# Kernel tuning notes

Hardware: AMD Instinct MI355X
Metric: run time of the kernel (lower is better)

## Reference

```python
import jax, jax.numpy as jnp
import numpy as np

B, S, D, E, K = 4, 2048, 1024, 8, 2
H = 4 * D  # FFN hidden per expert


def setup_inputs() -> dict:
    key = jax.random.key(0)
    ks = jax.random.split(key, 5)
    s = 0.02  # init scale
    return {
        "x": jax.random.normal(ks[0], (B, S, D), dtype=jnp.float32),
        "Wg": jax.random.normal(ks[1], (D, E), dtype=jnp.float32) * s,
        "bg": jnp.zeros((E,), dtype=jnp.float32),
        "W1": jax.random.normal(ks[2], (E, D, H), dtype=jnp.float32) * s,
        "b1": jnp.zeros((E, H), dtype=jnp.float32),
        "W2": jax.random.normal(ks[3], (E, H, D), dtype=jnp.float32) * s,
        "b2": jnp.zeros((E, D), dtype=jnp.float32),
    }


def reference(x, Wg, bg, W1, b1, W2, b2):
    # Router: softmax over expert logits, then top-k (torch.topk semantics)
    probs = jax.nn.softmax(x @ Wg + bg, axis=-1)      # [B,S,E]
    w, idx = jax.lax.top_k(probs, K)                   # [B,S,K] each
    # Dense all-experts MLP (matches original: every expert runs on every token)
    h = jax.nn.gelu(jnp.einsum('bsd,edh->bseh', x, W1) + b1, approximate=False)  # [B,S,E,H]
    y = jnp.einsum('bseh,ehd->bsed', h, W2) + b2       # [B,S,E,D]
    # One-hot mask + weighted sum == gather selected experts, scale by w, sum over k
    yk = jnp.take_along_axis(y, idx[..., None], axis=2)  # [B,S,K,D]
    return jnp.sum(yk * w[..., None], axis=2)            # [B,S,D]
```

## Files before the change

kernel.cpp:

```cpp
#include <hip/hip_runtime.h>
#include <hip/hip_bf16.h>
#include <math.h>


#define TOK     8192
#define DMODEL  1024
#define NEXP    8
#define HFF     4096
#define NASSIGN 16384
#define SLOTPAD 16512
#define BM      128
#define BN      128
#define BK      64
#define MAXRT   135

typedef __attribute__((ext_vector_type(8))) short s16x8;
typedef __attribute__((ext_vector_type(4))) float f32x4;

__device__ __forceinline__ void gll16(const void* g, void* l) {
  __builtin_amdgcn_global_load_lds((const __attribute__((address_space(1))) void*)g,
                                   (__attribute__((address_space(3))) void*)l, 16, 0, 0);
}

__global__ void transpose_cvt(const float* __restrict__ in, __hip_bfloat16* __restrict__ out,
                              int R, int C) {
  __shared__ float t[64][65];
  const float* src = in + (size_t)blockIdx.z * R * C;
  __hip_bfloat16* dst = out + (size_t)blockIdx.z * R * C;
  const int r0 = blockIdx.y * 64, c0 = blockIdx.x * 64;
  const int tc = threadIdx.x & 63, tr = threadIdx.x >> 6;
#pragma unroll
  for (int i = 0; i < 16; ++i) {
    int r = i * 4 + tr;
    t[r][tc] = src[(size_t)(r0 + r) * C + c0 + tc];
  }
  __syncthreads();
  const int jl = (threadIdx.x & 15) * 4;
  const int cw = threadIdx.x >> 4;
#pragma unroll
  for (int p = 0; p < 4; ++p) {
    const int cc = p * 16 + cw;
    union { ushort4 u; __hip_bfloat16 h[4]; } o;
#pragma unroll
    for (int u = 0; u < 4; ++u) o.h[u] = __float2bfloat16(t[jl + u][cc]);
    *(ushort4*)(dst + (size_t)(c0 + cc) * R + r0 + jl) = o.u;
  }
}

__global__ void router_kernel(const float* __restrict__ x, const float* __restrict__ Wg,
                              const float* __restrict__ bg, int* __restrict__ idx,
                              float* __restrict__ wtok, int* __restrict__ counts) {
  __shared__ int scnt[NEXP];
  if (threadIdx.x < NEXP) scnt[threadIdx.x] = 0;
  __syncthreads();
  const int wave = threadIdx.x >> 6, lane = threadIdx.x & 63;
  const int t = blockIdx.x * 4 + wave;
  float acc[NEXP];
#pragma unroll
  for (int e = 0; e < NEXP; ++e) acc[e] = 0.f;
  const float* xr = x + (size_t)t * DMODEL + lane * 16;
#pragma unroll
  for (int j = 0; j < 4; ++j) {
    float4 xv = *(const float4*)(xr + j * 4);
    const float* wr = Wg + (size_t)(lane * 16 + j * 4) * NEXP;
#pragma unroll
    for (int u = 0; u < 4; ++u) {
      float xs = (&xv.x)[u];
      float4 w0 = *(const float4*)(wr + u * NEXP);
      float4 w1 = *(const float4*)(wr + u * NEXP + 4);
      acc[0] += xs * w0.x; acc[1] += xs * w0.y; acc[2] += xs * w0.z; acc[3] += xs * w0.w;
      acc[4] += xs * w1.x; acc[5] += xs * w1.y; acc[6] += xs * w1.z; acc[7] += xs * w1.w;
    }
  }
#pragma unroll
  for (int off = 32; off >= 1; off >>= 1) {
#pragma unroll
    for (int e = 0; e < NEXP; ++e) acc[e] += __shfl_xor(acc[e], off, 64);
  }
  if (lane == 0) {
    float l[NEXP], m = -1e30f;
#pragma unroll
    for (int e = 0; e < NEXP; ++e) { l[e] = acc[e] + bg[e]; m = fmaxf(m, l[e]); }
    float p[NEXP], s = 0.f;
#pragma unroll
    for (int e = 0; e < NEXP; ++e) { p[e] = expf(l[e] - m); s += p[e]; }
    float inv = 1.f / s;
#pragma unroll
    for (int e = 0; e < NEXP; ++e) p[e] *= inv;
    int i0 = 0; float v0 = p[0];
#pragma unroll
    for (int e = 1; e < NEXP; ++e) if (p[e] > v0) { v0 = p[e]; i0 = e; }
    int i1 = -1; float v1 = -1e30f;
#pragma unroll
    for (int e = 0; e < NEXP; ++e) if (e != i0 && p[e] > v1) { v1 = p[e]; i1 = e; }
    idx[2 * t] = i0; idx[2 * t + 1] = i1;
    wtok[2 * t] = v0; wtok[2 * t + 1] = v1;
    atomicAdd(&scnt[i0], 1); atomicAdd(&scnt[i1], 1);
  }
  __syncthreads();
  if (threadIdx.x < NEXP) atomicAdd(&counts[threadIdx.x], scnt[threadIdx.x]);
}

__global__ void scan_kernel(int* ctrl) {
  if (threadIdx.x == 0 && blockIdx.x == 0) {
    int* counts = ctrl;
    int* cursor = ctrl + 8;
    int* expOff = ctrl + 16;
    int* tro = ctrl + 26;
    expOff[0] = 0; tro[0] = 0;
    for (int e = 0; e < NEXP; ++e) {
      expOff[e + 1] = expOff[e] + counts[e];
      tro[e + 1] = tro[e] + (counts[e] + BM - 1) / BM;
      cursor[e] = expOff[e];
    }
  }
}

__global__ void scatter_kernel(const int* __restrict__ idx, const float* __restrict__ wtok,
                               int* ctrl, int* __restrict__ perm, float* __restrict__ wslot) {
  __shared__ int lcnt[NEXP];
  __shared__ int lbase[NEXP];
  const int t = blockIdx.x * 256 + threadIdx.x;
  if (threadIdx.x < NEXP) lcnt[threadIdx.x] = 0;
  __syncthreads();
  const int e0 = idx[2 * t], e1 = idx[2 * t + 1];
  const int l0 = atomicAdd(&lcnt[e0], 1);
  const int l1 = atomicAdd(&lcnt[e1], 1);
  __syncthreads();
  if (threadIdx.x < NEXP)
    lbase[threadIdx.x] = atomicAdd(&ctrl[8 + threadIdx.x], lcnt[threadIdx.x]);
  __syncthreads();
  const int s0 = lbase[e0] + l0, s1 = lbase[e1] + l1;
  perm[s0] = t; perm[s1] = t;
  wslot[s0] = wtok[2 * t]; wslot[s1] = wtok[2 * t + 1];
}

__global__ void gather_cvt_x(const float* __restrict__ x, const int* __restrict__ perm,
                             __hip_bfloat16* __restrict__ xg) {
  const int slot = blockIdx.x;
  const int t = perm[slot];
  const float4 v = *(const float4*)(x + (size_t)t * DMODEL + threadIdx.x * 4);
  union { ushort4 u; __hip_bfloat16 h[4]; } o;
  o.h[0] = __float2bfloat16(v.x); o.h[1] = __float2bfloat16(v.y);
  o.h[2] = __float2bfloat16(v.z); o.h[3] = __float2bfloat16(v.w);
  *(ushort4*)(xg + (size_t)slot * DMODEL + threadIdx.x * 4) = o.u;
}


__global__ __launch_bounds__(256, 3) void gemm1_kernel(
    const __hip_bfloat16* __restrict__ xg, const __hip_bfloat16* __restrict__ w1t,
    const float* __restrict__ b1, __hip_bfloat16* __restrict__ hbuf,
    const int* __restrict__ ctrl) {
  const int* expOff = ctrl + 16;
  const int* tro = ctrl + 26;
  const int w = blockIdx.x;
  const int rt = w >> 5, nt = w & 31;
  if (rt >= tro[NEXP]) return;
  int e = 0;
#pragma unroll
  for (int q = 1; q < NEXP; ++q) if (tro[q] <= rt) e = q;
  const int rowBase = expOff[e] + (rt - tro[e]) * BM;
  const int rowEnd = expOff[e + 1];

  __shared__ __hip_bfloat16 lA[BM * BK];
  __shared__ __hip_bfloat16 lB[BN * BK];

  const int tid = threadIdx.x;
  const int lane = tid & 63, wave = tid >> 6;
  const int quad = lane >> 4, lm = lane & 15;
  const int waveM = (wave >> 1) * 64, waveN = (wave & 1) * 64;

  f32x4 acc[4][4];
#pragma unroll
  for (int a = 0; a < 4; ++a)
#pragma unroll
    for (int b = 0; b < 4; ++b) acc[a][b] = (f32x4){0.f, 0.f, 0.f, 0.f};

  const __hip_bfloat16* bbase = w1t + (size_t)e * HFF * DMODEL + (size_t)nt * BN * DMODEL;
  const __hip_bfloat16* gA[4]; const __hip_bfloat16* gB[4];
  __hip_bfloat16* sA[4]; __hip_bfloat16* sB[4];
#pragma unroll
  for (int i = 0; i < 4; ++i) {
    const int s = tid + 256 * i;
    const int r = s >> 3, sl = s & 7, kc = sl ^ (r & 7);
    gA[i] = xg + (size_t)(rowBase + r) * DMODEL + kc * 8;
    gB[i] = bbase + (size_t)r * DMODEL + kc * 8;
    sA[i] = lA + s * 8; sB[i] = lB + s * 8;
  }

  int aOff[4], bOff[4];
#pragma unroll
  for (int tm = 0; tm < 4; ++tm) {
    int r = waveM + tm * 16 + lm;
    aOff[tm] = r * 64 + (quad ^ (r & 7)) * 8;
  }
#pragma unroll
  for (int tn = 0; tn < 4; ++tn) {
    int r = waveN + tn * 16 + lm;
    bOff[tn] = r * 64 + (quad ^ (r & 7)) * 8;
  }

  for (int kt = 0; kt < DMODEL / BK; ++kt) {
#pragma unroll
    for (int i = 0; i < 4; ++i) { gll16(gA[i], sA[i]); gll16(gB[i], sB[i]); }
#pragma unroll
    for (int i = 0; i < 4; ++i) { gA[i] += BK; gB[i] += BK; }
    __syncthreads();
#pragma unroll
    for (int h = 0; h < 2; ++h) {
      s16x8 af[4], bfr[4];
#pragma unroll
      for (int tm = 0; tm < 4; ++tm) af[tm] = *(const s16x8*)(lA + (aOff[tm] ^ (h * 32)));
#pragma unroll
      for (int tn = 0; tn < 4; ++tn) bfr[tn] = *(const s16x8*)(lB + (bOff[tn] ^ (h * 32)));
#pragma unroll
      for (int tm = 0; tm < 4; ++tm)
#pragma unroll
        for (int tn = 0; tn < 4; ++tn)
          acc[tm][tn] = __builtin_amdgcn_mfma_f32_16x16x32_bf16(af[tm], bfr[tn], acc[tm][tn], 0, 0, 0);
    }
    __syncthreads();
  }

  const int colBase = nt * BN + waveN;
  float bv[4];
#pragma unroll
  for (int tn = 0; tn < 4; ++tn) bv[tn] = b1[e * HFF + colBase + tn * 16 + lm];
#pragma unroll
  for (int tm = 0; tm < 4; ++tm) {
    const int rb = rowBase + waveM + tm * 16 + quad * 4;
#pragma unroll
    for (int reg = 0; reg < 4; ++reg) {
      const int row = rb + reg;
      if (row < rowEnd) {
#pragma unroll
        for (int tn = 0; tn < 4; ++tn) {
          float v = acc[tm][tn][reg] + bv[tn];
          v = 0.5f * v * (1.f + erff(v * 0.70710678118654752f));
          hbuf[(size_t)row * HFF + colBase + tn * 16 + lm] = __float2bfloat16(v);
        }
      }
    }
  }
}

__global__ __launch_bounds__(256, 3) void gemm2_kernel(
    const __hip_bfloat16* __restrict__ hbuf, const __hip_bfloat16* __restrict__ w2t,
    const float* __restrict__ b2, const float* __restrict__ wslot,
    const int* __restrict__ perm, float* __restrict__ out, const int* __restrict__ ctrl) {
  const int* expOff = ctrl + 16;
  const int* tro = ctrl + 26;
  const int w = blockIdx.x;
  const int rt = w >> 3, nt = w & 7;
  if (rt >= tro[NEXP]) return;
  int e = 0;
#pragma unroll
  for (int q = 1; q < NEXP; ++q) if (tro[q] <= rt) e = q;
  const int rowBase = expOff[e] + (rt - tro[e]) * BM;
  const int rowEnd = expOff[e + 1];

  __shared__ __hip_bfloat16 lA[BM * BK];
  __shared__ __hip_bfloat16 lB[BN * BK];

  const int tid = threadIdx.x;
  const int lane = tid & 63, wave = tid >> 6;
  const int quad = lane >> 4, lm = lane & 15;
  const int waveM = (wave >> 1) * 64, waveN = (wave & 1) * 64;

  f32x4 acc[4][4];
#pragma unroll
  for (int a = 0; a < 4; ++a)
#pragma unroll
    for (int b = 0; b < 4; ++b) acc[a][b] = (f32x4){0.f, 0.f, 0.f, 0.f};

  const __hip_bfloat16* bbase = w2t + (size_t)e * DMODEL * HFF + (size_t)nt * BN * HFF;
  const __hip_bfloat16* gA[4]; const __hip_bfloat16* gB[4];
  __hip_bfloat16* sA[4]; __hip_bfloat16* sB[4];
#pragma unroll
  for (int i = 0; i < 4; ++i) {
    const int s = tid + 256 * i;
    const int r = s >> 3, sl = s & 7, kc = sl ^ (r & 7);
    gA[i] = hbuf + (size_t)(rowBase + r) * HFF + kc * 8;
    gB[i] = bbase + (size_t)r * HFF + kc * 8;
    sA[i] = lA + s * 8; sB[i] = lB + s * 8;
  }

  int aOff[4], bOff[4];
#pragma unroll
  for (int tm = 0; tm < 4; ++tm) {
    int r = waveM + tm * 16 + lm;
    aOff[tm] = r * 64 + (quad ^ (r & 7)) * 8;
  }
#pragma unroll
  for (int tn = 0; tn < 4; ++tn) {
    int r = waveN + tn * 16 + lm;
    bOff[tn] = r * 64 + (quad ^ (r & 7)) * 8;
  }

  for (int kt = 0; kt < HFF / BK; ++kt) {
#pragma unroll
    for (int i = 0; i < 4; ++i) { gll16(gA[i], sA[i]); gll16(gB[i], sB[i]); }
#pragma unroll
    for (int i = 0; i < 4; ++i) { gA[i] += BK; gB[i] += BK; }
    __syncthreads();
#pragma unroll
    for (int h = 0; h < 2; ++h) {
      s16x8 af[4], bfr[4];
#pragma unroll
      for (int tm = 0; tm < 4; ++tm) af[tm] = *(const s16x8*)(lA + (aOff[tm] ^ (h * 32)));
#pragma unroll
      for (int tn = 0; tn < 4; ++tn) bfr[tn] = *(const s16x8*)(lB + (bOff[tn] ^ (h * 32)));
#pragma unroll
      for (int tm = 0; tm < 4; ++tm)
#pragma unroll
        for (int tn = 0; tn < 4; ++tn)
          acc[tm][tn] = __builtin_amdgcn_mfma_f32_16x16x32_bf16(af[tm], bfr[tn], acc[tm][tn], 0, 0, 0);
    }
    __syncthreads();
  }

  const int colBase = nt * BN + waveN;
  float bv[4];
#pragma unroll
  for (int tn = 0; tn < 4; ++tn) bv[tn] = b2[e * DMODEL + colBase + tn * 16 + lm];
#pragma unroll
  for (int tm = 0; tm < 4; ++tm) {
    const int rb = rowBase + waveM + tm * 16 + quad * 4;
#pragma unroll
    for (int reg = 0; reg < 4; ++reg) {
      const int row = rb + reg;
      if (row < rowEnd) {
        const float wr = wslot[row];
        float* orow = out + (size_t)perm[row] * DMODEL + colBase;
#pragma unroll
        for (int tn = 0; tn < 4; ++tn)
          atomicAdd(orow + tn * 16 + lm, (acc[tm][tn][reg] + bv[tn]) * wr);
      }
    }
  }
}

extern "C" void kernel_launch(void* const* d_in, const int* in_sizes, int n_in,
                              void* d_out, int out_size, void* d_ws, size_t ws_size,
                              hipStream_t stream) {
  const float* x  = (const float*)d_in[0];
  const float* Wg = (const float*)d_in[1];
  const float* bg = (const float*)d_in[2];
  const float* W1 = (const float*)d_in[3];
  const float* b1 = (const float*)d_in[4];
  const float* W2 = (const float*)d_in[5];
  const float* b2 = (const float*)d_in[6];
  float* out = (float*)d_out;

  char* ws = (char*)d_ws;
  size_t off = 0;
  auto take = [&](size_t bytes) -> char* {
    char* p = ws + off;
    off = (off + bytes + 255) & ~(size_t)255;
    return p;
  };
  int*   ctrl  = (int*)take(64 * sizeof(int));
  int*   idx   = (int*)take((size_t)TOK * 2 * 4);
  float* wtok  = (float*)take((size_t)TOK * 2 * 4);
  int*   perm  = (int*)take((size_t)SLOTPAD * 4);
  float* wslot = (float*)take((size_t)SLOTPAD * 4);
  __hip_bfloat16* W1t = (__hip_bfloat16*)take((size_t)NEXP * HFF * DMODEL * 2);
  __hip_bfloat16* W2t = (__hip_bfloat16*)take((size_t)NEXP * DMODEL * HFF * 2);
  __hip_bfloat16* xgb = (__hip_bfloat16*)take((size_t)SLOTPAD * DMODEL * 2);
  __hip_bfloat16* hb  = (__hip_bfloat16*)take((size_t)SLOTPAD * HFF * 2);
  (void)ws_size; (void)in_sizes; (void)n_in; (void)out_size;

  hipMemsetAsync(ctrl, 0, 64 * sizeof(int), stream);
  hipMemsetAsync(out, 0, (size_t)TOK * DMODEL * 4, stream);
  transpose_cvt<<<dim3(HFF / 64, DMODEL / 64, NEXP), 256, 0, stream>>>(W1, W1t, DMODEL, HFF);
  transpose_cvt<<<dim3(DMODEL / 64, HFF / 64, NEXP), 256, 0, stream>>>(W2, W2t, HFF, DMODEL);
  router_kernel<<<TOK / 4, 256, 0, stream>>>(x, Wg, bg, idx, wtok, ctrl);
  scan_kernel<<<1, 64, 0, stream>>>(ctrl);
  scatter_kernel<<<TOK / 256, 256, 0, stream>>>(idx, wtok, ctrl, perm, wslot);
  gather_cvt_x<<<NASSIGN, 256, 0, stream>>>(x, perm, xgb);
  gemm1_kernel<<<MAXRT * (HFF / BN), 256, 0, stream>>>(xgb, W1t, b1, hb, ctrl);
  gemm2_kernel<<<MAXRT * (DMODEL / BN), 256, 0, stream>>>(hb, W2t, b2, wslot, perm, out, ctrl);
}
```

Measured before the change: 793.5 us.

## Double-buffer GEMM LDS tiles, fuse launches, replace atomic combine with gather

Both grouped GEMMs now double-buffer their LDS tiles. The next K-tile is prefetched while MFMAs run on the current one, with one barrier per iteration and raised wave priority during the MFMA burst. The two weight transposes merge into one launch, and the scan is folded into the router through a last-block-done counter. Gemm2 now writes weighted per-slot rows to a scratch buffer that aliases W1t, and a new combine kernel sums the two slots per token. This removes the output memset and the float atomics. It costs extra LDS (occupancy bound drops to 2) plus an extra pass over the slot outputs.

Result: slower. 982.0 us (+23.8%).

```diff
diff --git a/kernel.cpp b/kernel.cpp
--- a/kernel.cpp
+++ b/kernel.cpp
@@ -22,12 +22,21 @@
                                    (__attribute__((address_space(3))) void*)l, 16, 0, 0);
 }
 
-__global__ void transpose_cvt(const float* __restrict__ in, __hip_bfloat16* __restrict__ out,
-                              int R, int C) {
+__global__ void transpose_cvt(const float* __restrict__ W1, const float* __restrict__ W2,
+                              __hip_bfloat16* __restrict__ W1t, __hip_bfloat16* __restrict__ W2t) {
   __shared__ float t[64][65];
-  const float* src = in + (size_t)blockIdx.z * R * C;
-  __hip_bfloat16* dst = out + (size_t)blockIdx.z * R * C;
-  const int r0 = blockIdx.y * 64, c0 = blockIdx.x * 64;
+  const int z = blockIdx.y;
+  const float* src; __hip_bfloat16* dst; int R, C, bx, by;
+  if (z < 8) {
+    R = DMODEL; C = HFF;
+    src = W1 + (size_t)z * R * C; dst = W1t + (size_t)z * R * C;
+    bx = blockIdx.x & 63; by = blockIdx.x >> 6;
+  } else {
+    R = HFF; C = DMODEL;
+    src = W2 + (size_t)(z - 8) * R * C; dst = W2t + (size_t)(z - 8) * R * C;
+    bx = blockIdx.x & 15; by = blockIdx.x >> 4;
+  }
+  const int r0 = by * 64, c0 = bx * 64;
   const int tc = threadIdx.x & 63, tr = threadIdx.x >> 6;
 #pragma unroll
   for (int i = 0; i < 16; ++i) {
@@ -49,7 +58,7 @@
 
 __global__ void router_kernel(const float* __restrict__ x, const float* __restrict__ Wg,
                               const float* __restrict__ bg, int* __restrict__ idx,
-                              float* __restrict__ wtok, int* __restrict__ counts) {
+                              float* __restrict__ wtok, int* ctrl) {
   __shared__ int scnt[NEXP];
   if (threadIdx.x < NEXP) scnt[threadIdx.x] = 0;
   __syncthreads();
@@ -98,26 +107,30 @@
     atomicAdd(&scnt[i0], 1); atomicAdd(&scnt[i1], 1);
   }
   __syncthreads();
-  if (threadIdx.x < NEXP) atomicAdd(&counts[threadIdx.x], scnt[threadIdx.x]);
-}
-
-__global__ void scan_kernel(int* ctrl) {
-  if (threadIdx.x == 0 && blockIdx.x == 0) {
-    int* counts = ctrl;
-    int* cursor = ctrl + 8;
-    int* expOff = ctrl + 16;
-    int* tro = ctrl + 26;
-    expOff[0] = 0; tro[0] = 0;
-    for (int e = 0; e < NEXP; ++e) {
-      expOff[e + 1] = expOff[e] + counts[e];
-      tro[e + 1] = tro[e] + (counts[e] + BM - 1) / BM;
-      cursor[e] = expOff[e];
+  if (threadIdx.x < NEXP) atomicAdd(&ctrl[threadIdx.x], scnt[threadIdx.x]);
+  if (threadIdx.x == 0) {
+    __threadfence();
+    const int done = atomicAdd(&ctrl[63], 1);
+    if (done == (int)gridDim.x - 1) {
+      int c[NEXP];
+#pragma unroll
+      for (int e = 0; e < NEXP; ++e) c[e] = atomicAdd(&ctrl[e], 0);
+      int eo = 0, tr = 0;
+      ctrl[16] = 0; ctrl[26] = 0;
+#pragma unroll
+      for (int e = 0; e < NEXP; ++e) {
+        ctrl[8 + e] = eo;
+        eo += c[e]; tr += (c[e] + BM - 1) / BM;
+        ctrl[17 + e] = eo;
+        ctrl[27 + e] = tr;
+      }
     }
   }
 }
 
 __global__ void scatter_kernel(const int* __restrict__ idx, const float* __restrict__ wtok,
-                               int* ctrl, int* __restrict__ perm, float* __restrict__ wslot) {
+                               int* ctrl, int* __restrict__ perm, int* __restrict__ ts,
+                               float* __restrict__ wslot) {
   __shared__ int lcnt[NEXP];
   __shared__ int lbase[NEXP];
   const int t = blockIdx.x * 256 + threadIdx.x;
@@ -132,6 +145,7 @@
   __syncthreads();
   const int s0 = lbase[e0] + l0, s1 = lbase[e1] + l1;
   perm[s0] = t; perm[s1] = t;
+  ts[2 * t] = s0; ts[2 * t + 1] = s1;
   wslot[s0] = wtok[2 * t]; wslot[s1] = wtok[2 * t + 1];
 }
 
@@ -147,7 +161,7 @@
 }
 
 
-__global__ __launch_bounds__(256, 3) void gemm1_kernel(
+__global__ __launch_bounds__(256, 2) void gemm1_kernel(
     const __hip_bfloat16* __restrict__ xg, const __hip_bfloat16* __restrict__ w1t,
     const float* __restrict__ b1, __hip_bfloat16* __restrict__ hbuf,
     const int* __restrict__ ctrl) {
@@ -162,8 +176,8 @@
   const int rowBase = expOff[e] + (rt - tro[e]) * BM;
   const int rowEnd = expOff[e + 1];
 
-  __shared__ __hip_bfloat16 lA[BM * BK];
-  __shared__ __hip_bfloat16 lB[BN * BK];
+  __shared__ __hip_bfloat16 lA[2 * BM * BK];
+  __shared__ __hip_bfloat16 lB[2 * BN * BK];
 
   const int tid = threadIdx.x;
   const int lane = tid & 63, wave = tid >> 6;
@@ -178,14 +192,12 @@
 
   const __hip_bfloat16* bbase = w1t + (size_t)e * HFF * DMODEL + (size_t)nt * BN * DMODEL;
   const __hip_bfloat16* gA[4]; const __hip_bfloat16* gB[4];
-  __hip_bfloat16* sA[4]; __hip_bfloat16* sB[4];
 #pragma unroll
   for (int i = 0; i < 4; ++i) {
     const int s = tid + 256 * i;
     const int r = s >> 3, sl = s & 7, kc = sl ^ (r & 7);
     gA[i] = xg + (size_t)(rowBase + r) * DMODEL + kc * 8;
     gB[i] = bbase + (size_t)r * DMODEL + kc * 8;
-    sA[i] = lA + s * 8; sB[i] = lB + s * 8;
   }
 
   int aOff[4], bOff[4];
@@ -200,26 +212,46 @@
     bOff[tn] = r * 64 + (quad ^ (r & 7)) * 8;
   }
 
-  for (int kt = 0; kt < DMODEL / BK; ++kt) {
-#pragma unroll
-    for (int i = 0; i < 4; ++i) { gll16(gA[i], sA[i]); gll16(gB[i], sB[i]); }
-#pragma unroll
-    for (int i = 0; i < 4; ++i) { gA[i] += BK; gB[i] += BK; }
-    __syncthreads();
+#pragma unroll
+  for (int i = 0; i < 4; ++i) {
+    gll16(gA[i], lA + tid * 8 + i * 2048);
+    gll16(gB[i], lB + tid * 8 + i * 2048);
+    gA[i] += BK; gB[i] += BK;
+  }
+  __syncthreads();
+
+  const int NTI = DMODEL / BK;
+  for (int kt = 0; kt < NTI; ++kt) {
+    if (kt + 1 < NTI) {
+      const int nb = (kt + 1) & 1;
+#pragma unroll
+      for (int i = 0; i < 4; ++i) {
+        gll16(gA[i], lA + nb * 8192 + tid * 8 + i * 2048);
+        gll16(gB[i], lB + nb * 8192 + tid * 8 + i * 2048);
+        gA[i] += BK; gB[i] += BK;
+      }
+    }
+    const __hip_bfloat16* ba = lA + (kt & 1) * 8192;
+    const __hip_bfloat16* bb = lB + (kt & 1) * 8192;
+    s16x8 af[2][4], bfr[2][4];
 #pragma unroll
     for (int h = 0; h < 2; ++h) {
-      s16x8 af[4], bfr[4];
-#pragma unroll
-      for (int tm = 0; tm < 4; ++tm) af[tm] = *(const s16x8*)(lA + (aOff[tm] ^ (h * 32)));
-#pragma unroll
-      for (int tn = 0; tn < 4; ++tn) bfr[tn] = *(const s16x8*)(lB + (bOff[tn] ^ (h * 32)));
+#pragma unroll
+      for (int tm = 0; tm < 4; ++tm) af[h][tm] = *(const s16x8*)(ba + (aOff[tm] ^ (h * 32)));
+#pragma unroll
+      for (int tn = 0; tn < 4; ++tn) bfr[h][tn] = *(const s16x8*)(bb + (bOff[tn] ^ (h * 32)));
+    }
+    __builtin_amdgcn_s_setprio(1);
+#pragma unroll
+    for (int h = 0; h < 2; ++h)
 #pragma unroll
       for (int tm = 0; tm < 4; ++tm)
 #pragma unroll
         for (int tn = 0; tn < 4; ++tn)
-          acc[tm][tn] = __builtin_amdgcn_mfma_f32_16x16x32_bf16(af[tm], bfr[tn], acc[tm][tn], 0, 0, 0);
-    }
-    __syncthreads();
+          acc[tm][tn] = __builtin_amdgcn_mfma_f32_16x16x32_bf16(af[h][tm], bfr[h][tn],
+                                                                acc[tm][tn], 0, 0, 0);
+    __builtin_amdgcn_s_setprio(0);
+    if (kt + 1 < NTI) __syncthreads();
   }
 
   const int colBase = nt * BN + waveN;
@@ -244,10 +276,10 @@
   }
 }
 
-__global__ __launch_bounds__(256, 3) void gemm2_kernel(
+__global__ __launch_bounds__(256, 2) void gemm2_kernel(
     const __hip_bfloat16* __restrict__ hbuf, const __hip_bfloat16* __restrict__ w2t,
     const float* __restrict__ b2, const float* __restrict__ wslot,
-    const int* __restrict__ perm, float* __restrict__ out, const int* __restrict__ ctrl) {
+    float* __restrict__ y, const int* __restrict__ ctrl) {
   const int* expOff = ctrl + 16;
   const int* tro = ctrl + 26;
   const int w = blockIdx.x;
@@ -259,8 +291,8 @@
   const int rowBase = expOff[e] + (rt - tro[e]) * BM;
   const int rowEnd = expOff[e + 1];
 
-  __shared__ __hip_bfloat16 lA[BM * BK];
-  __shared__ __hip_bfloat16 lB[BN * BK];
+  __shared__ __hip_bfloat16 lA[2 * BM * BK];
+  __shared__ __hip_bfloat16 lB[2 * BN * BK];
 
   const int tid = threadIdx.x;
   const int lane = tid & 63, wave = tid >> 6;
@@ -275,14 +307,12 @@
 
   const __hip_bfloat16* bbase = w2t + (size_t)e * DMODEL * HFF + (size_t)nt * BN * HFF;
   const __hip_bfloat16* gA[4]; const __hip_bfloat16* gB[4];
-  __hip_bfloat16* sA[4]; __hip_bfloat16* sB[4];
 #pragma unroll
   for (int i = 0; i < 4; ++i) {
     const int s = tid + 256 * i;
     const int r = s >> 3, sl = s & 7, kc = sl ^ (r & 7);
     gA[i] = hbuf + (size_t)(rowBase + r) * HFF + kc * 8;
     gB[i] = bbase + (size_t)r * HFF + kc * 8;
-    sA[i] = lA + s * 8; sB[i] = lB + s * 8;
   }
 
   int aOff[4], bOff[4];
@@ -297,26 +327,46 @@
     bOff[tn] = r * 64 + (quad ^ (r & 7)) * 8;
   }
 
-  for (int kt = 0; kt < HFF / BK; ++kt) {
-#pragma unroll
-    for (int i = 0; i < 4; ++i) { gll16(gA[i], sA[i]); gll16(gB[i], sB[i]); }
-#pragma unroll
-    for (int i = 0; i < 4; ++i) { gA[i] += BK; gB[i] += BK; }
-    __syncthreads();
+#pragma unroll
+  for (int i = 0; i < 4; ++i) {
+    gll16(gA[i], lA + tid * 8 + i * 2048);
+    gll16(gB[i], lB + tid * 8 + i * 2048);
+    gA[i] += BK; gB[i] += BK;
+  }
+  __syncthreads();
+
+  const int NTI = HFF / BK;
+  for (int kt = 0; kt < NTI; ++kt) {
+    if (kt + 1 < NTI) {
+      const int nb = (kt + 1) & 1;
+#pragma unroll
+      for (int i = 0; i < 4; ++i) {
+        gll16(gA[i], lA + nb * 8192 + tid * 8 + i * 2048);
+        gll16(gB[i], lB + nb * 8192 + tid * 8 + i * 2048);
+        gA[i] += BK; gB[i] += BK;
+      }
+    }
+    const __hip_bfloat16* ba = lA + (kt & 1) * 8192;
+    const __hip_bfloat16* bb = lB + (kt & 1) * 8192;
+    s16x8 af[2][4], bfr[2][4];
 #pragma unroll
     for (int h = 0; h < 2; ++h) {
-      s16x8 af[4], bfr[4];
-#pragma unroll
-      for (int tm = 0; tm < 4; ++tm) af[tm] = *(const s16x8*)(lA + (aOff[tm] ^ (h * 32)));
-#pragma unroll
-      for (int tn = 0; tn < 4; ++tn) bfr[tn] = *(const s16x8*)(lB + (bOff[tn] ^ (h * 32)));
+#pragma unroll
+      for (int tm = 0; tm < 4; ++tm) af[h][tm] = *(const s16x8*)(ba + (aOff[tm] ^ (h * 32)));
+#pragma unroll
+      for (int tn = 0; tn < 4; ++tn) bfr[h][tn] = *(const s16x8*)(bb + (bOff[tn] ^ (h * 32)));
+    }
+    __builtin_amdgcn_s_setprio(1);
+#pragma unroll
+    for (int h = 0; h < 2; ++h)
 #pragma unroll
       for (int tm = 0; tm < 4; ++tm)
 #pragma unroll
         for (int tn = 0; tn < 4; ++tn)
-          acc[tm][tn] = __builtin_amdgcn_mfma_f32_16x16x32_bf16(af[tm], bfr[tn], acc[tm][tn], 0, 0, 0);
-    }
-    __syncthreads();
+          acc[tm][tn] = __builtin_amdgcn_mfma_f32_16x16x32_bf16(af[h][tm], bfr[h][tn],
+                                                                acc[tm][tn], 0, 0, 0);
+    __builtin_amdgcn_s_setprio(0);
+    if (kt + 1 < NTI) __syncthreads();
   }
 
   const int colBase = nt * BN + waveN;
@@ -331,13 +381,24 @@
       const int row = rb + reg;
       if (row < rowEnd) {
         const float wr = wslot[row];
-        float* orow = out + (size_t)perm[row] * DMODEL + colBase;
+        float* yr = y + (size_t)row * DMODEL + colBase;
 #pragma unroll
         for (int tn = 0; tn < 4; ++tn)
-          atomicAdd(orow + tn * 16 + lm, (acc[tm][tn][reg] + bv[tn]) * wr);
+          yr[tn * 16 + lm] = (acc[tm][tn][reg] + bv[tn]) * wr;
       }
     }
   }
+}
+
+__global__ void combine_kernel(const float* __restrict__ y, const int* __restrict__ ts,
+                               float* __restrict__ out) {
+  const int t = blockIdx.x;
+  const int s0 = ts[2 * t], s1 = ts[2 * t + 1];
+  const int c = threadIdx.x * 4;
+  const float4 a = *(const float4*)(y + (size_t)s0 * DMODEL + c);
+  const float4 b = *(const float4*)(y + (size_t)s1 * DMODEL + c);
+  float4 r; r.x = a.x + b.x; r.y = a.y + b.y; r.z = a.z + b.z; r.w = a.w + b.w;
+  *(float4*)(out + (size_t)t * DMODEL + c) = r;
 }
 
 extern "C" void kernel_launch(void* const* d_in, const int* in_sizes, int n_in,
@@ -363,21 +424,21 @@
   int*   idx   = (int*)take((size_t)TOK * 2 * 4);
   float* wtok  = (float*)take((size_t)TOK * 2 * 4);
   int*   perm  = (int*)take((size_t)SLOTPAD * 4);
+  int*   ts    = (int*)take((size_t)TOK * 2 * 4);
   float* wslot = (float*)take((size_t)SLOTPAD * 4);
   __hip_bfloat16* W1t = (__hip_bfloat16*)take((size_t)NEXP * HFF * DMODEL * 2);
   __hip_bfloat16* W2t = (__hip_bfloat16*)take((size_t)NEXP * DMODEL * HFF * 2);
   __hip_bfloat16* xgb = (__hip_bfloat16*)take((size_t)SLOTPAD * DMODEL * 2);
   __hip_bfloat16* hb  = (__hip_bfloat16*)take((size_t)SLOTPAD * HFF * 2);
+  float* y = (float*)W1t;
   (void)ws_size; (void)in_sizes; (void)n_in; (void)out_size;
 
   hipMemsetAsync(ctrl, 0, 64 * sizeof(int), stream);
-  hipMemsetAsync(out, 0, (size_t)TOK * DMODEL * 4, stream);
-  transpose_cvt<<<dim3(HFF / 64, DMODEL / 64, NEXP), 256, 0, stream>>>(W1, W1t, DMODEL, HFF);
-  transpose_cvt<<<dim3(DMODEL / 64, HFF / 64, NEXP), 256, 0, stream>>>(W2, W2t, HFF, DMODEL);
+  transpose_cvt<<<dim3(1024, 16), 256, 0, stream>>>(W1, W2, W1t, W2t);
   router_kernel<<<TOK / 4, 256, 0, stream>>>(x, Wg, bg, idx, wtok, ctrl);
-  scan_kernel<<<1, 64, 0, stream>>>(ctrl);
-  scatter_kernel<<<TOK / 256, 256, 0, stream>>>(idx, wtok, ctrl, perm, wslot);
+  scatter_kernel<<<TOK / 256, 256, 0, stream>>>(idx, wtok, ctrl, perm, ts, wslot);
   gather_cvt_x<<<NASSIGN, 256, 0, stream>>>(x, perm, xgb);
   gemm1_kernel<<<MAXRT * (HFF / BN), 256, 0, stream>>>(xgb, W1t, b1, hb, ctrl);
-  gemm2_kernel<<<MAXRT * (DMODEL / BN), 256, 0, stream>>>(hb, W2t, b2, wslot, perm, out, ctrl);
-}
+  gemm2_kernel<<<MAXRT * (DMODEL / BN), 256, 0, stream>>>(hb, W2t, b2, wslot, y, ctrl);
+  combine_kernel<<<TOK, 256, 0, stream>>>(y, ts, out);
+}
```
